# Performance work log

Hardware: AMD Instinct MI355X
Metric: run time of the kernel (lower is better)

## Reference

```python
import jax, jax.numpy as jnp
import numpy as np

N = 50000
NEG_SLOPE = 0.2


def gat_conv(x, src, dst, W, a_src, a_dst, b):
    # PyG GATConv, heads=1: h = xW; e_ij = LeakyReLU(a_src.h_j + a_dst.h_i);
    # softmax over edges sharing destination i; out_i = sum_j alpha_ij h_j + b.
    h = x @ W                                   # [N, F]
    as_ = h @ a_src                             # [N]
    ad_ = h @ a_dst                             # [N]
    e = jax.nn.leaky_relu(as_[src] + ad_[dst], NEG_SLOPE)  # [E]
    m = jax.ops.segment_max(e, dst, num_segments=N)        # per-dst max
    m = jnp.where(jnp.isfinite(m), m, 0.0)
    p = jnp.exp(e - m[dst])
    denom = jax.ops.segment_sum(p, dst, num_segments=N)
    alpha = p / jnp.maximum(denom[dst], 1e-16)             # [E]
    out = jax.ops.segment_sum(alpha[:, None] * h[src], dst, num_segments=N)
    return out + b


def setup_inputs() -> dict:
    key = jax.random.key(0)
    ks = jax.random.split(key, 12)
    E, L = 800000, 262144
    F_in, F_mid, F_out = 128, 64, 32
    x = jax.random.normal(ks[0], (N, F_in), dtype=jnp.float32)
    edge_index = jax.random.randint(ks[1], (2, E), 0, N, dtype=jnp.int32)
    edge_label_index = jax.random.randint(ks[2], (2, L), 0, N, dtype=jnp.int32)
    s1 = 1.0 / np.sqrt(F_in)
    s2 = 1.0 / np.sqrt(F_mid)
    return {
        "x": x,
        "edge_index": edge_index,
        "edge_label_index": edge_label_index,
        "W1": jax.random.normal(ks[3], (F_in, F_mid), jnp.float32) * s1,
        "a_src1": jax.random.normal(ks[4], (F_mid,), jnp.float32) * s2,
        "a_dst1": jax.random.normal(ks[5], (F_mid,), jnp.float32) * s2,
        "b1": jnp.zeros((F_mid,), jnp.float32),
        "W2": jax.random.normal(ks[6], (F_mid, F_out), jnp.float32) * s2,
        "a_src2": jax.random.normal(ks[7], (F_out,), jnp.float32) * (1.0 / np.sqrt(F_out)),
        "a_dst2": jax.random.normal(ks[8], (F_out,), jnp.float32) * (1.0 / np.sqrt(F_out)),
        "b2": jnp.zeros((F_out,), jnp.float32),
    }


def reference(x, edge_index, edge_label_index, W1, a_src1, a_dst1, b1, W2, a_src2, a_dst2, b2):
    # add self-loops (PyG GATConv default add_self_loops=True)
    loops = jnp.arange(N, dtype=edge_index.dtype)
    src = jnp.concatenate([edge_index[0], loops])
    dst = jnp.concatenate([edge_index[1], loops])
    z = jax.nn.relu(gat_conv(x, src, dst, W1, a_src1, a_dst1, b1))
    z = gat_conv(z, src, dst, W2, a_src2, a_dst2, b2)
    # dot-product decode over candidate edges
    return jnp.sum(z[edge_label_index[0]] * z[edge_label_index[1]], axis=-1)
```

## Files before the change

kernel.cpp:

```cpp
#include <hip/hip_runtime.h>

#define NN 50000
#define NEG 0.2f
#define NBUCK 196
#define NBLK 208

__device__ __forceinline__ float leaky(float v) { return v > 0.0f ? v : NEG * v; }

__device__ __forceinline__ unsigned f2bf(float x) {
    unsigned u = __float_as_uint(x);
    return (u + 0x7FFFu + ((u >> 16) & 1u)) >> 16;
}

__global__ __launch_bounds__(256) void k_hist_gemm1(
        const int* __restrict__ ei, int E, int T, int CHUNK,
        int* __restrict__ bh,
        const float* __restrict__ x, const float* __restrict__ W,
        const float* __restrict__ a_src, const float* __restrict__ a_dst,
        unsigned int* __restrict__ hu, float* __restrict__ as_, float* __restrict__ ad_) {
    __shared__ float xs[4][8][128];
    __shared__ int hist[NBUCK];
    int tid = threadIdx.x;
    if (blockIdx.x < NBLK) {
        if (tid < NBUCK) hist[tid] = 0;
        __syncthreads();
        int beg = blockIdx.x * CHUNK;
        int end = min(beg + CHUNK, T);
        for (int i = beg + tid; i < end; i += 256) {
            int dv = (i < E) ? ei[E + i] : (i - E);
            atomicAdd(&hist[dv >> 8], 1);
        }
        __syncthreads();
        if (tid < NBUCK) bh[blockIdx.x * NBUCK + tid] = hist[tid];
        return;
    }
    int gblock = blockIdx.x - NBLK;
    int wl = tid >> 6;
    int lane = tid & 63;
    int base = (gblock * 4 + wl) * 8;
    if (base >= NN) return;
#pragma unroll
    for (int n = 0; n < 8; ++n) {
        int node = base + n;
        xs[wl][n][lane]      = x[node * 128 + lane];
        xs[wl][n][lane + 64] = x[node * 128 + 64 + lane];
    }
    float acc[8] = {0, 0, 0, 0, 0, 0, 0, 0};
#pragma unroll 8
    for (int kg = 0; kg < 32; ++kg) {
        float w0 = W[(4 * kg + 0) * 64 + lane];
        float w1 = W[(4 * kg + 1) * 64 + lane];
        float w2 = W[(4 * kg + 2) * 64 + lane];
        float w3 = W[(4 * kg + 3) * 64 + lane];
#pragma unroll
        for (int n = 0; n < 8; ++n) {
            float4 xv = *(const float4*)&xs[wl][n][kg * 4];
            acc[n] = fmaf(xv.x, w0, fmaf(xv.y, w1, fmaf(xv.z, w2, fmaf(xv.w, w3, acc[n]))));
        }
    }
    float pa = a_src[lane], pd = a_dst[lane];
#pragma unroll
    for (int n = 0; n < 8; ++n) {
        int node = base + n;
        unsigned my = f2bf(acc[n]);
        unsigned nb = __shfl_down(my, 1, 64);
        if ((lane & 1) == 0) hu[node * 32 + (lane >> 1)] = my | (nb << 16);
        float s = acc[n] * pa;
        float d = acc[n] * pd;
#pragma unroll
        for (int off = 32; off > 0; off >>= 1) {
            s += __shfl_xor(s, off, 64);
            d += __shfl_xor(d, off, 64);
        }
        if (lane == 0) { as_[node] = s; ad_[node] = d; }
    }
}

__global__ __launch_bounds__(256) void k_scan_col(int* __restrict__ bh,
                                                  int* __restrict__ btot) {
    int k = blockIdx.x;
    int tid = threadIdx.x;
    __shared__ int wsum[4];
    int v = (tid < NBLK) ? bh[tid * NBUCK + k] : 0;
    int lane = tid & 63, w = tid >> 6;
    int inc = v;
#pragma unroll
    for (int off = 1; off < 64; off <<= 1) {
        int t = __shfl_up(inc, off, 64);
        if (lane >= off) inc += t;
    }
    if (lane == 63) wsum[w] = inc;
    __syncthreads();
    int wpre = 0;
    for (int q = 0; q < w; ++q) wpre += wsum[q];
    int excl = wpre + inc - v;
    if (tid < NBLK) bh[tid * NBUCK + k] = excl;
    if (tid == 255) btot[k] = wpre + inc;
}

__global__ __launch_bounds__(256) void k_scan_base(const int* __restrict__ btot,
                                                   int* __restrict__ bucket_base) {
    int tid = threadIdx.x;
    __shared__ int wsum[4];
    int v = (tid < NBUCK) ? btot[tid] : 0;
    int lane = tid & 63, w = tid >> 6;
    int inc = v;
#pragma unroll
    for (int off = 1; off < 64; off <<= 1) {
        int t = __shfl_up(inc, off, 64);
        if (lane >= off) inc += t;
    }
    if (lane == 63) wsum[w] = inc;
    __syncthreads();
    int wpre = 0;
    for (int q = 0; q < w; ++q) wpre += wsum[q];
    int excl = wpre + inc - v;
    if (tid < NBUCK) bucket_base[tid] = excl;
    if (tid == 255) bucket_base[NBUCK] = wsum[0] + wsum[1] + wsum[2] + wsum[3];
}

__global__ __launch_bounds__(256) void k_part(
        const int* __restrict__ ei, int E, int T, int CHUNK,
        const int* __restrict__ bh, const int* __restrict__ bucket_base,
        unsigned int* __restrict__ part) {
    __shared__ int cur[NBUCK];
    int tid = threadIdx.x;
    if (tid < NBUCK) cur[tid] = bucket_base[tid] + bh[blockIdx.x * NBUCK + tid];
    __syncthreads();
    int beg = blockIdx.x * CHUNK;
    int end = min(beg + CHUNK, T);
    for (int i = beg + tid; i < end; i += 256) {
        int sv, dv;
        if (i < E) { sv = ei[i]; dv = ei[E + i]; }
        else { sv = dv = i - E; }
        int pos = atomicAdd(&cur[dv >> 8], 1);
        part[pos] = (unsigned)sv | ((unsigned)(dv & 255) << 16);
    }
}

__global__ __launch_bounds__(256) void k_csr(
        const unsigned int* __restrict__ part, const int* __restrict__ bucket_base,
        int* __restrict__ row_start, int* __restrict__ cnt,
        unsigned short* __restrict__ csr_src) {
    int k = blockIdx.x;
    int tid = threadIdx.x;
    int beg = bucket_base[k], end = bucket_base[k + 1];
    __shared__ int hist[256], roff[256], wsum[4];
    hist[tid] = 0;
    __syncthreads();
    for (int i = beg + tid; i < end; i += 256)
        atomicAdd(&hist[part[i] >> 16], 1);
    __syncthreads();
    int lane = tid & 63, w = tid >> 6;
    int v = hist[tid];
    int inc = v;
#pragma unroll
    for (int off = 1; off < 64; off <<= 1) {
        int t = __shfl_up(inc, off, 64);
        if (lane >= off) inc += t;
    }
    if (lane == 63) wsum[w] = inc;
    __syncthreads();
    int wpre = 0;
    for (int q = 0; q < w; ++q) wpre += wsum[q];
    int excl = wpre + inc - v;
    roff[tid] = beg + excl;
    int dst = (k << 8) + tid;
    if (dst < NN) { row_start[dst] = beg + excl; cnt[dst] = v; }
    __syncthreads();
    for (int i = beg + tid; i < end; i += 256) {
        unsigned int e = part[i];
        int pos = atomicAdd(&roff[e >> 16], 1);
        csr_src[pos] = (unsigned short)(e & 0xFFFFu);
    }
}

__global__ void k_aggr1(const int* __restrict__ row_start, const int* __restrict__ cnt,
                        const unsigned short* __restrict__ csr_src,
                        const float* __restrict__ as_, const float* __restrict__ ad_,
                        const unsigned int* __restrict__ hu, const float* __restrict__ b,
                        float* __restrict__ out) {
    int gid = blockIdx.x * blockDim.x + threadIdx.x;
    int dst = gid >> 5;
    int f = gid & 31;
    if (dst >= NN) return;
    int start = row_start[dst];
    int deg = cnt[dst];
    float ad = ad_[dst];
    float ssum, ax = 0.0f, ay = 0.0f;

    if (deg <= 32) {
        int sj = 0;
        float ej = -1e30f;
        if (f < deg) {
            sj = csr_src[start + f];
            ej = leaky(as_[sj] + ad);
        }
        float m = ej;
#pragma unroll
        for (int off = 16; off > 0; off >>= 1) m = fmaxf(m, __shfl_xor(m, off, 32));
        float pj = (f < deg) ? __expf(ej - m) : 0.0f;
        ssum = pj;
#pragma unroll
        for (int off = 16; off > 0; off >>= 1) ssum += __shfl_xor(ssum, off, 32);
        int t = 0;
        for (; t + 4 <= deg; t += 4) {
            int s0 = __shfl(sj, t, 32), s1 = __shfl(sj, t + 1, 32);
            int s2 = __shfl(sj, t + 2, 32), s3 = __shfl(sj, t + 3, 32);
            float p0 = __shfl(pj, t, 32), p1 = __shfl(pj, t + 1, 32);
            float p2 = __shfl(pj, t + 2, 32), p3 = __shfl(pj, t + 3, 32);
            unsigned g0 = hu[s0 * 32 + f];
            unsigned g1 = hu[s1 * 32 + f];
            unsigned g2 = hu[s2 * 32 + f];
            unsigned g3 = hu[s3 * 32 + f];
            ax = fmaf(p0, __uint_as_float(g0 << 16), ax);
            ay = fmaf(p0, __uint_as_float(g0 & 0xFFFF0000u), ay);
            ax = fmaf(p1, __uint_as_float(g1 << 16), ax);
            ay = fmaf(p1, __uint_as_float(g1 & 0xFFFF0000u), ay);
            ax = fmaf(p2, __uint_as_float(g2 << 16), ax);
            ay = fmaf(p2, __uint_as_float(g2 & 0xFFFF0000u), ay);
            ax = fmaf(p3, __uint_as_float(g3 << 16), ax);
            ay = fmaf(p3, __uint_as_float(g3 & 0xFFFF0000u), ay);
        }
        for (; t < deg; ++t) {
            int sv = __shfl(sj, t, 32);
            float pv = __shfl(pj, t, 32);
            unsigned g = hu[sv * 32 + f];
            ax = fmaf(pv, __uint_as_float(g << 16), ax);
            ay = fmaf(pv, __uint_as_float(g & 0xFFFF0000u), ay);
        }
    } else {
        float m = -1e30f;
        for (int base = 0; base < deg; base += 32) {
            int j = base + f;
            if (j < deg) m = fmaxf(m, leaky(as_[csr_src[start + j]] + ad));
        }
#pragma unroll
        for (int off = 16; off > 0; off >>= 1) m = fmaxf(m, __shfl_xor(m, off, 32));
        ssum = 0.0f;
        for (int base = 0; base < deg; base += 32) {
            int j = base + f;
            int sj = 0;
            float pj = 0.0f;
            if (j < deg) {
                sj = csr_src[start + j];
                pj = __expf(leaky(as_[sj] + ad) - m);
            }
            ssum += pj;
            int lim = min(32, deg - base);
            for (int t = 0; t < lim; ++t) {
                int sv = __shfl(sj, t, 32);
                float pv = __shfl(pj, t, 32);
                unsigned g = hu[sv * 32 + f];
                ax = fmaf(pv, __uint_as_float(g << 16), ax);
                ay = fmaf(pv, __uint_as_float(g & 0xFFFF0000u), ay);
            }
        }
#pragma unroll
        for (int off = 16; off > 0; off >>= 1) ssum += __shfl_xor(ssum, off, 32);
    }

    float inv = 1.0f / ssum;
    float2 bb = *(const float2*)&b[2 * f];
    float2 r;
    r.x = fmaxf(ax * inv + bb.x, 0.0f);
    r.y = fmaxf(ay * inv + bb.y, 0.0f);
    *(float2*)&out[dst * 64 + 2 * f] = r;
}

__global__ __launch_bounds__(256) void k_gemm2(
        const float* __restrict__ z, const float* __restrict__ W,
        const float* __restrict__ a_src, const float* __restrict__ a_dst,
        float* __restrict__ h, float* __restrict__ as_, float* __restrict__ ad_) {
    int wave = (blockIdx.x * blockDim.x + threadIdx.x) >> 6;
    int lane = threadIdx.x & 63;
    int g = lane >> 5;
    int f = lane & 31;
    int wl = threadIdx.x >> 6;
    __shared__ float zs[4][16][64];
    int base = wave * 16;
    if (base >= NN) return;
#pragma unroll
    for (int n = 0; n < 16; ++n) zs[wl][n][lane] = z[(base + n) * 64 + lane];
    float wreg[32];
#pragma unroll
    for (int kk = 0; kk < 32; ++kk) wreg[kk] = W[(g * 32 + kk) * 32 + f];
    float pa = a_src[f], pd = a_dst[f];
#pragma unroll 4
    for (int n = 0; n < 16; ++n) {
        int node = base + n;
        float part = 0.0f;
#pragma unroll
        for (int kg = 0; kg < 8; ++kg) {
            float4 zv = *(const float4*)&zs[wl][n][g * 32 + kg * 4];
            part = fmaf(zv.x, wreg[4 * kg + 0],
                   fmaf(zv.y, wreg[4 * kg + 1],
                   fmaf(zv.z, wreg[4 * kg + 2],
                   fmaf(zv.w, wreg[4 * kg + 3], part))));
        }
        float hv = part + __shfl_xor(part, 32, 64);
        if (g == 0) h[node * 32 + f] = hv;
        float s = hv * pa, d = hv * pd;
#pragma unroll
        for (int off = 16; off > 0; off >>= 1) {
            s += __shfl_xor(s, off, 64);
            d += __shfl_xor(d, off, 64);
        }
        if (lane == 0) { as_[node] = s; ad_[node] = d; }
    }
}

__global__ void k_aggr2(const int* __restrict__ row_start, const int* __restrict__ cnt,
                        const unsigned short* __restrict__ csr_src,
                        const float* __restrict__ as_, const float* __restrict__ ad_,
                        const float* __restrict__ h, const float* __restrict__ b,
                        float* __restrict__ out) {
    const int F = 32;
    int gid = blockIdx.x * blockDim.x + threadIdx.x;
    int dst = gid / F;
    int f = gid % F;
    if (dst >= NN) return;
    int start = row_start[dst];
    int deg = cnt[dst];
    float ad = ad_[dst];
    float ssum, acc = 0.0f;

    if (deg <= F) {
        int sj = 0;
        float ej = -1e30f;
        if (f < deg) {
            sj = csr_src[start + f];
            ej = leaky(as_[sj] + ad);
        }
        float m = ej;
#pragma unroll
        for (int off = F / 2; off > 0; off >>= 1) m = fmaxf(m, __shfl_xor(m, off, F));
        float pj = (f < deg) ? __expf(ej - m) : 0.0f;
        ssum = pj;
#pragma unroll
        for (int off = F / 2; off > 0; off >>= 1) ssum += __shfl_xor(ssum, off, F);
        int t = 0;
        for (; t + 4 <= deg; t += 4) {
            int s0 = __shfl(sj, t, F), s1 = __shfl(sj, t + 1, F);
            int s2 = __shfl(sj, t + 2, F), s3 = __shfl(sj, t + 3, F);
            float p0 = __shfl(pj, t, F), p1 = __shfl(pj, t + 1, F);
            float p2 = __shfl(pj, t + 2, F), p3 = __shfl(pj, t + 3, F);
            float g0 = h[s0 * F + f];
            float g1 = h[s1 * F + f];
            float g2 = h[s2 * F + f];
            float g3 = h[s3 * F + f];
            acc = fmaf(p0, g0, acc);
            acc = fmaf(p1, g1, acc);
            acc = fmaf(p2, g2, acc);
            acc = fmaf(p3, g3, acc);
        }
        for (; t < deg; ++t) {
            int sv = __shfl(sj, t, F);
            float pv = __shfl(pj, t, F);
            acc = fmaf(pv, h[sv * F + f], acc);
        }
    } else {
        float m = -1e30f;
        for (int base = 0; base < deg; base += F) {
            int j = base + f;
            if (j < deg) m = fmaxf(m, leaky(as_[csr_src[start + j]] + ad));
        }
#pragma unroll
        for (int off = F / 2; off > 0; off >>= 1) m = fmaxf(m, __shfl_xor(m, off, F));
        ssum = 0.0f;
        for (int base = 0; base < deg; base += F) {
            int j = base + f;
            int sj = 0;
            float pj = 0.0f;
            if (j < deg) {
                sj = csr_src[start + j];
                pj = __expf(leaky(as_[sj] + ad) - m);
            }
            ssum += pj;
            int lim = min(F, deg - base);
            for (int t = 0; t < lim; ++t) {
                int sv = __shfl(sj, t, F);
                float pv = __shfl(pj, t, F);
                acc = fmaf(pv, h[sv * F + f], acc);
            }
        }
#pragma unroll
        for (int off = F / 2; off > 0; off >>= 1) ssum += __shfl_xor(ssum, off, F);
    }

    out[dst * F + f] = acc / ssum + b[f];
}

__global__ void k_decode(const int* __restrict__ eli, int L,
                         const float* __restrict__ z2, float* __restrict__ out) {
    int gid = blockIdx.x * blockDim.x + threadIdx.x;
    int pair = gid >> 3;
    int f4 = gid & 7;
    if (pair >= L) return;
    int i = eli[pair];
    int j = eli[L + pair];
    float4 a = *(const float4*)&z2[i * 32 + f4 * 4];
    float4 b = *(const float4*)&z2[j * 32 + f4 * 4];
    float v = a.x * b.x + a.y * b.y + a.z * b.z + a.w * b.w;
#pragma unroll
    for (int off = 4; off > 0; off >>= 1) v += __shfl_xor(v, off, 8);
    if (f4 == 0) out[pair] = v;
}

extern "C" void kernel_launch(void* const* d_in, const int* in_sizes, int n_in,
                              void* d_out, int out_size, void* d_ws, size_t ws_size,
                              hipStream_t stream) {
    const float* x     = (const float*)d_in[0];
    const int*   ei    = (const int*)d_in[1];
    const int*   eli   = (const int*)d_in[2];
    const float* W1    = (const float*)d_in[3];
    const float* asrc1 = (const float*)d_in[4];
    const float* adst1 = (const float*)d_in[5];
    const float* b1    = (const float*)d_in[6];
    const float* W2    = (const float*)d_in[7];
    const float* asrc2 = (const float*)d_in[8];
    const float* adst2 = (const float*)d_in[9];
    const float* b2    = (const float*)d_in[10];
    float* out = (float*)d_out;

    const int E = in_sizes[1] / 2;
    const int L = in_sizes[2] / 2;
    const int T = E + NN;
    const int CHUNK = (T + NBLK - 1) / NBLK;

    float* ws  = (float*)d_ws;
    unsigned int* hu = (unsigned int*)ws;
    float* h2  = (float*)(hu + NN * 32);
    float* z1  = h2 + NN * 32;
    float* z2  = z1 + NN * 64;
    float* as1 = z2 + NN * 32;
    float* ad1 = as1 + NN;
    float* as2 = ad1 + NN;
    float* ad2 = as2 + NN;
    int* row_start   = (int*)(ad2 + NN);
    int* cnt         = row_start + NN;
    int* bucket_base = cnt + NN;
    int* btot        = bucket_base + NBUCK + 1;
    int* bh          = btot + NBUCK;
    unsigned int*   part    = (unsigned int*)(bh + NBLK * NBUCK);
    unsigned short* csr_src = (unsigned short*)(part + T);

    const int GB = (NN / 8 + 3) / 4;

    k_hist_gemm1<<<NBLK + GB, 256, 0, stream>>>(ei, E, T, CHUNK, bh,
                                                x, W1, asrc1, adst1, hu, as1, ad1);
    k_scan_col<<<NBUCK, 256, 0, stream>>>(bh, btot);
    k_scan_base<<<1, 256, 0, stream>>>(btot, bucket_base);
    k_part<<<NBLK, 256, 0, stream>>>(ei, E, T, CHUNK, bh, bucket_base, part);
    k_csr<<<NBUCK, 256, 0, stream>>>(part, bucket_base, row_start, cnt, csr_src);

    k_aggr1<<<(NN * 32 + 255) / 256, 256, 0, stream>>>(
        row_start, cnt, csr_src, as1, ad1, hu, b1, z1);

    k_gemm2<<<(NN / 16 + 3) / 4, 256, 0, stream>>>(z1, W2, asrc2, adst2, h2, as2, ad2);
    k_aggr2<<<(NN * 32 + 255) / 256, 256, 0, stream>>>(
        row_start, cnt, csr_src, as2, ad2, h2, b2, z2);

    k_decode<<<(L * 8 + 255) / 256, 256, 0, stream>>>(eli, L, z2, out);
}
```

Baseline: 221.9 us.

## Store layer-2 features as bf16, fold bucket scan into partition kernels, pack row info

The layer-2 GEMM now writes its transformed features as packed bf16 pairs, so the per-edge gather in the second aggregation reads half the bytes. The separate single-block bucket-base scan kernel is removed: k_part recomputes the exclusive scan of bucket totals itself, and k_csr derives its bucket range by reducing the totals of earlier buckets. Row start and degree are packed into one int2 per node so each aggregation thread loads them together. This cuts one launch and some gather traffic, at the cost of reduced precision in layer-2 features and redundant scan work in every block.

Measured after the change: 219.2 us. Within noise of the previous version (-1.2%).

```diff
diff --git a/kernel.cpp b/kernel.cpp
--- a/kernel.cpp
+++ b/kernel.cpp
@@ -10,6 +10,9 @@
 __device__ __forceinline__ unsigned f2bf(float x) {
     unsigned u = __float_as_uint(x);
     return (u + 0x7FFFu + ((u >> 16) & 1u)) >> 16;
+}
+__device__ __forceinline__ float bf2f(unsigned short u) {
+    return __uint_as_float(((unsigned)u) << 16);
 }
 
 __global__ __launch_bounds__(256) void k_hist_gemm1(
@@ -98,10 +101,13 @@
     if (tid == 255) btot[k] = wpre + inc;
 }
 
-__global__ __launch_bounds__(256) void k_scan_base(const int* __restrict__ btot,
-                                                   int* __restrict__ bucket_base) {
+__global__ __launch_bounds__(256) void k_part(
+        const int* __restrict__ ei, int E, int T, int CHUNK,
+        const int* __restrict__ bh, const int* __restrict__ btot,
+        unsigned int* __restrict__ part) {
+    __shared__ int cur[NBUCK];
+    __shared__ int wsum[4];
     int tid = threadIdx.x;
-    __shared__ int wsum[4];
     int v = (tid < NBUCK) ? btot[tid] : 0;
     int lane = tid & 63, w = tid >> 6;
     int inc = v;
@@ -114,18 +120,7 @@
     __syncthreads();
     int wpre = 0;
     for (int q = 0; q < w; ++q) wpre += wsum[q];
-    int excl = wpre + inc - v;
-    if (tid < NBUCK) bucket_base[tid] = excl;
-    if (tid == 255) bucket_base[NBUCK] = wsum[0] + wsum[1] + wsum[2] + wsum[3];
-}
-
-__global__ __launch_bounds__(256) void k_part(
-        const int* __restrict__ ei, int E, int T, int CHUNK,
-        const int* __restrict__ bh, const int* __restrict__ bucket_base,
-        unsigned int* __restrict__ part) {
-    __shared__ int cur[NBUCK];
-    int tid = threadIdx.x;
-    if (tid < NBUCK) cur[tid] = bucket_base[tid] + bh[blockIdx.x * NBUCK + tid];
+    if (tid < NBUCK) cur[tid] = (wpre + inc - v) + bh[blockIdx.x * NBUCK + tid];
     __syncthreads();
     int beg = blockIdx.x * CHUNK;
     int end = min(beg + CHUNK, T);
@@ -139,19 +134,25 @@
 }
 
 __global__ __launch_bounds__(256) void k_csr(
-        const unsigned int* __restrict__ part, const int* __restrict__ bucket_base,
-        int* __restrict__ row_start, int* __restrict__ cnt,
-        unsigned short* __restrict__ csr_src) {
+        const unsigned int* __restrict__ part, const int* __restrict__ btot,
+        int2* __restrict__ rc, unsigned short* __restrict__ csr_src) {
     int k = blockIdx.x;
     int tid = threadIdx.x;
-    int beg = bucket_base[k], end = bucket_base[k + 1];
     __shared__ int hist[256], roff[256], wsum[4];
+    int lane = tid & 63, w = tid >> 6;
+    {
+        int v = (tid < k) ? btot[tid] : 0;
+#pragma unroll
+        for (int off = 32; off > 0; off >>= 1) v += __shfl_xor(v, off, 64);
+        if (lane == 0) wsum[w] = v;
+    }
     hist[tid] = 0;
     __syncthreads();
+    int beg = wsum[0] + wsum[1] + wsum[2] + wsum[3];
+    int end = beg + btot[k];
     for (int i = beg + tid; i < end; i += 256)
         atomicAdd(&hist[part[i] >> 16], 1);
     __syncthreads();
-    int lane = tid & 63, w = tid >> 6;
     int v = hist[tid];
     int inc = v;
 #pragma unroll
@@ -159,6 +160,7 @@
         int t = __shfl_up(inc, off, 64);
         if (lane >= off) inc += t;
     }
+    __syncthreads();
     if (lane == 63) wsum[w] = inc;
     __syncthreads();
     int wpre = 0;
@@ -166,7 +168,7 @@
     int excl = wpre + inc - v;
     roff[tid] = beg + excl;
     int dst = (k << 8) + tid;
-    if (dst < NN) { row_start[dst] = beg + excl; cnt[dst] = v; }
+    if (dst < NN) rc[dst] = make_int2(beg + excl, v);
     __syncthreads();
     for (int i = beg + tid; i < end; i += 256) {
         unsigned int e = part[i];
@@ -175,7 +177,7 @@
     }
 }
 
-__global__ void k_aggr1(const int* __restrict__ row_start, const int* __restrict__ cnt,
+__global__ void k_aggr1(const int2* __restrict__ rc,
                         const unsigned short* __restrict__ csr_src,
                         const float* __restrict__ as_, const float* __restrict__ ad_,
                         const unsigned int* __restrict__ hu, const float* __restrict__ b,
@@ -184,8 +186,9 @@
     int dst = gid >> 5;
     int f = gid & 31;
     if (dst >= NN) return;
-    int start = row_start[dst];
-    int deg = cnt[dst];
+    int2 rcv = rc[dst];
+    int start = rcv.x;
+    int deg = rcv.y;
     float ad = ad_[dst];
     float ssum, ax = 0.0f, ay = 0.0f;
 
@@ -271,7 +274,7 @@
 __global__ __launch_bounds__(256) void k_gemm2(
         const float* __restrict__ z, const float* __restrict__ W,
         const float* __restrict__ a_src, const float* __restrict__ a_dst,
-        float* __restrict__ h, float* __restrict__ as_, float* __restrict__ ad_) {
+        unsigned int* __restrict__ hu2, float* __restrict__ as_, float* __restrict__ ad_) {
     int wave = (blockIdx.x * blockDim.x + threadIdx.x) >> 6;
     int lane = threadIdx.x & 63;
     int g = lane >> 5;
@@ -299,7 +302,9 @@
                    fmaf(zv.w, wreg[4 * kg + 3], part))));
         }
         float hv = part + __shfl_xor(part, 32, 64);
-        if (g == 0) h[node * 32 + f] = hv;
+        unsigned my = f2bf(hv);
+        unsigned nb = __shfl_down(my, 1, 64);
+        if (g == 0 && (f & 1) == 0) hu2[node * 16 + (f >> 1)] = my | (nb << 16);
         float s = hv * pa, d = hv * pd;
 #pragma unroll
         for (int off = 16; off > 0; off >>= 1) {
@@ -310,18 +315,19 @@
     }
 }
 
-__global__ void k_aggr2(const int* __restrict__ row_start, const int* __restrict__ cnt,
+__global__ void k_aggr2(const int2* __restrict__ rc,
                         const unsigned short* __restrict__ csr_src,
                         const float* __restrict__ as_, const float* __restrict__ ad_,
-                        const float* __restrict__ h, const float* __restrict__ b,
+                        const unsigned short* __restrict__ h2u, const float* __restrict__ b,
                         float* __restrict__ out) {
     const int F = 32;
     int gid = blockIdx.x * blockDim.x + threadIdx.x;
     int dst = gid / F;
     int f = gid % F;
     if (dst >= NN) return;
-    int start = row_start[dst];
-    int deg = cnt[dst];
+    int2 rcv = rc[dst];
+    int start = rcv.x;
+    int deg = rcv.y;
     float ad = ad_[dst];
     float ssum, acc = 0.0f;
 
@@ -345,10 +351,10 @@
             int s2 = __shfl(sj, t + 2, F), s3 = __shfl(sj, t + 3, F);
             float p0 = __shfl(pj, t, F), p1 = __shfl(pj, t + 1, F);
             float p2 = __shfl(pj, t + 2, F), p3 = __shfl(pj, t + 3, F);
-            float g0 = h[s0 * F + f];
-            float g1 = h[s1 * F + f];
-            float g2 = h[s2 * F + f];
-            float g3 = h[s3 * F + f];
+            float g0 = bf2f(h2u[s0 * F + f]);
+            float g1 = bf2f(h2u[s1 * F + f]);
+            float g2 = bf2f(h2u[s2 * F + f]);
+            float g3 = bf2f(h2u[s3 * F + f]);
             acc = fmaf(p0, g0, acc);
             acc = fmaf(p1, g1, acc);
             acc = fmaf(p2, g2, acc);
@@ -357,7 +363,7 @@
         for (; t < deg; ++t) {
             int sv = __shfl(sj, t, F);
             float pv = __shfl(pj, t, F);
-            acc = fmaf(pv, h[sv * F + f], acc);
+            acc = fmaf(pv, bf2f(h2u[sv * F + f]), acc);
         }
     } else {
         float m = -1e30f;
@@ -381,7 +387,7 @@
             for (int t = 0; t < lim; ++t) {
                 int sv = __shfl(sj, t, F);
                 float pv = __shfl(pj, t, F);
-                acc = fmaf(pv, h[sv * F + f], acc);
+                acc = fmaf(pv, bf2f(h2u[sv * F + f]), acc);
             }
         }
 #pragma unroll
@@ -429,18 +435,16 @@
     const int CHUNK = (T + NBLK - 1) / NBLK;
 
     float* ws  = (float*)d_ws;
-    unsigned int* hu = (unsigned int*)ws;
-    float* h2  = (float*)(hu + NN * 32);
-    float* z1  = h2 + NN * 32;
+    unsigned int* hu  = (unsigned int*)ws;
+    unsigned int* hu2 = hu + NN * 32;
+    float* z1  = (float*)(hu2 + NN * 16);
     float* z2  = z1 + NN * 64;
     float* as1 = z2 + NN * 32;
     float* ad1 = as1 + NN;
     float* as2 = ad1 + NN;
     float* ad2 = as2 + NN;
-    int* row_start   = (int*)(ad2 + NN);
-    int* cnt         = row_start + NN;
-    int* bucket_base = cnt + NN;
-    int* btot        = bucket_base + NBUCK + 1;
+    int2* rc         = (int2*)(ad2 + NN);
+    int* btot        = (int*)(rc + NN);
     int* bh          = btot + NBUCK;
     unsigned int*   part    = (unsigned int*)(bh + NBLK * NBUCK);
     unsigned short* csr_src = (unsigned short*)(part + T);
@@ -450,16 +454,15 @@
     k_hist_gemm1<<<NBLK + GB, 256, 0, stream>>>(ei, E, T, CHUNK, bh,
                                                 x, W1, asrc1, adst1, hu, as1, ad1);
     k_scan_col<<<NBUCK, 256, 0, stream>>>(bh, btot);
-    k_scan_base<<<1, 256, 0, stream>>>(btot, bucket_base);
-    k_part<<<NBLK, 256, 0, stream>>>(ei, E, T, CHUNK, bh, bucket_base, part);
-    k_csr<<<NBUCK, 256, 0, stream>>>(part, bucket_base, row_start, cnt, csr_src);
+    k_part<<<NBLK, 256, 0, stream>>>(ei, E, T, CHUNK, bh, btot, part);
+    k_csr<<<NBUCK, 256, 0, stream>>>(part, btot, rc, csr_src);
 
     k_aggr1<<<(NN * 32 + 255) / 256, 256, 0, stream>>>(
-        row_start, cnt, csr_src, as1, ad1, hu, b1, z1);
-
-    k_gemm2<<<(NN / 16 + 3) / 4, 256, 0, stream>>>(z1, W2, asrc2, adst2, h2, as2, ad2);
+        rc, csr_src, as1, ad1, hu, b1, z1);
+
+    k_gemm2<<<(NN / 16 + 3) / 4, 256, 0, stream>>>(z1, W2, asrc2, adst2, hu2, as2, ad2);
     k_aggr2<<<(NN * 32 + 255) / 256, 256, 0, stream>>>(
-        row_start, cnt, csr_src, as2, ad2, h2, b2, z2);
+        rc, csr_src, as2, ad2, (const unsigned short*)hu2, b2, z2);
 
     k_decode<<<(L * 8 + 255) / 256, 256, 0, stream>>>(eli, L, z2, out);
 }
```
